# Performance work log

Measured on AMD Instinct MI355X. Metric: run time of the kernel, lower is better.

The kernel has to match this reference:

```python
import jax, jax.numpy as jnp
import numpy as np

FRAC_BITS = 16            # fixed-point fractional bits (MPC fixedpoint precision)
SCALE = float(1 << FRAC_BITS)

def fxp(v):
    """Emulate dup_with_precision: round value to the fixed-point grid with
    FRAC_BITS fractional bits. Straight-through (identity) gradient, matching
    the MPC backward pass which propagates gradients through truncation."""
    return v + jax.lax.stop_gradient(jnp.round(v * SCALE) / SCALE - v)


def setup_inputs() -> dict:
    key = jax.random.key(0)
    kx, kw = jax.random.split(key)
    in_dim, out_dim, batch = 4096, 4096, 2048
    x = jax.random.normal(kx, (batch, in_dim), dtype=jnp.float32)
    # Dense_Local init: w ~ N(0, 1/sqrt(in_dim+1)), b = zeros
    w = jax.random.normal(kw, (in_dim, out_dim), dtype=jnp.float32) / np.sqrt(in_dim + 1)
    b = jnp.zeros((out_dim,), dtype=jnp.float32)
    return {"x": x, "w": w, "b": b}


def reference(x, w, b):
    # quantize operands to the fixed-point grid (values live on the grid in MPC)
    xq = fxp(x)
    wq = fxp(w)
    # y = x @ w, then dup_with_precision(x.fixedpoint): truncate product back
    y = fxp(jnp.matmul(xq, wq))           # [batch, out_dim]
    # + bias
    y = y + fxp(b)
    # secure ReLU: s = drelu_local(y) (sign bit), y = relu(y, s) = y * s
    s = y >= 0
    y = jnp.where(s, y, jnp.zeros((), dtype=y.dtype))
    # final dup_with_precision(new_fixedpoint=x.fixedpoint)
    return fxp(y)
```

## Files before the change

### kernel.cpp

```cpp
#include <hip/hip_runtime.h>
#include <hip/hip_bf16.h>
#include <stdint.h>

#define M_DIM 2048
#define N_DIM 4096
#define K_DIM 4096

#define NT 64

typedef short short8 __attribute__((ext_vector_type(8)));
typedef float f32x4 __attribute__((ext_vector_type(4)));

typedef __attribute__((address_space(1))) unsigned int gu32;
typedef __attribute__((address_space(3))) unsigned int lu32;

__device__ static inline unsigned short f32_to_bf16(float f) {
  union { float f; unsigned int u; } v; v.f = f;
  unsigned int u = v.u;
  u += 0x7FFFu + ((u >> 16) & 1u);
  return (unsigned short)(u >> 16);
}

__global__ void cvt_x_kernel(const float* __restrict__ in, unsigned short* __restrict__ out) {
  size_t i = ((size_t)blockIdx.x * blockDim.x + threadIdx.x) * 8;
  f32x4 a = *(const f32x4*)(in + i);
  f32x4 b = *(const f32x4*)(in + i + 4);
  short8 o;
  o[0] = (short)f32_to_bf16(a[0]); o[1] = (short)f32_to_bf16(a[1]);
  o[2] = (short)f32_to_bf16(a[2]); o[3] = (short)f32_to_bf16(a[3]);
  o[4] = (short)f32_to_bf16(b[0]); o[5] = (short)f32_to_bf16(b[1]);
  o[6] = (short)f32_to_bf16(b[2]); o[7] = (short)f32_to_bf16(b[3]);
  *(short8*)(out + i) = o;
}

__global__ void transpose_cvt_w_kernel(const float* __restrict__ w, unsigned short* __restrict__ wt) {
  __shared__ unsigned short tile[64][64 + 8];
  int bn = blockIdx.x * 64;
  int bk = blockIdx.y * 64;
  int t = threadIdx.x;
  int c4 = (t & 15) * 4;
  int r0 = t >> 4;
#pragma unroll
  for (int p = 0; p < 4; ++p) {
    int r = r0 + p * 16;
    f32x4 v = *(const f32x4*)(w + (size_t)(bk + r) * N_DIM + bn + c4);
    tile[c4 + 0][r] = f32_to_bf16(v[0]);
    tile[c4 + 1][r] = f32_to_bf16(v[1]);
    tile[c4 + 2][r] = f32_to_bf16(v[2]);
    tile[c4 + 3][r] = f32_to_bf16(v[3]);
  }
  __syncthreads();
  int orow = t >> 2;
  int oc = (t & 3) * 16;
  short8 lo, hi;
#pragma unroll
  for (int j = 0; j < 8; ++j) {
    lo[j] = (short)tile[orow][oc + j];
    hi[j] = (short)tile[orow][oc + 8 + j];
  }
  unsigned short* op = wt + (size_t)(bn + orow) * K_DIM + bk + oc;
  *(short8*)(op) = lo;
  *(short8*)(op + 8) = hi;
}


__global__ __launch_bounds__(512) void gemm8_kernel(
    const unsigned short* __restrict__ A, const unsigned short* __restrict__ Bt,
    const float* __restrict__ bias, float* __restrict__ C) {
  __shared__ unsigned short sm16[3 * 24576];
  char* smem = (char*)&sm16[0];

  const int tid = threadIdx.x;
  const int lane = tid & 63;
  const int w = tid >> 6;
  const int wm = w >> 2, wn = w & 3;

  const int id = blockIdx.x;
  const int x = id & 7, j = id >> 3;
  const int by = ((x >> 2) << 3) + (j >> 2);
  const int bx = ((x & 3) << 2) + (j & 3);
  const int r0 = by * 128, c0 = bx * 256;

  const int l8 = lane >> 3, l7 = lane & 7;
  const int chunkE = ((l7 ^ (l8 & 7)) << 3);
  const unsigned short* Ag = A + (size_t)(r0 + w * 16 + l8) * K_DIM + chunkE;
  const unsigned short* Bg = Bt + (size_t)(c0 + w * 32 + l8) * K_DIM + chunkE;
  const int aL0 = w * 2048;
  const int bL0 = 16384 + w * 4096;

#define GL(gp, ldsoff) __builtin_amdgcn_global_load_lds((gu32*)(gp), (lu32*)(smem + (ldsoff)), 16, 0, 0)
#define STAGE_ALL(t, sb)                                               \
  do {                                                                 \
    GL(Ag + (size_t)(t) * 64, (sb) + aL0);                             \
    GL(Ag + (size_t)(t) * 64 + 8 * (size_t)K_DIM, (sb) + aL0 + 1024);  \
    GL(Bg + (size_t)(t) * 64, (sb) + bL0);                             \
    GL(Bg + (size_t)(t) * 64 + 8 * (size_t)K_DIM, (sb) + bL0 + 1024);  \
    GL(Bg + (size_t)(t) * 64 + 16 * (size_t)K_DIM, (sb) + bL0 + 2048); \
    GL(Bg + (size_t)(t) * 64 + 24 * (size_t)K_DIM, (sb) + bL0 + 3072); \
  } while (0)

  const int l15 = lane & 15, hi = lane >> 4;
  const int aR = (wm * 64 + l15) * 64;
  const int bR = 8192 + (wn * 64 + l15) * 64;
  const int slot0 = ((hi ^ l7) << 3);
  const int slot1 = (((4 + hi) ^ l7) << 3);

  f32x4 acc[4][4] = {};

  STAGE_ALL(0, 0);
  STAGE_ALL(1, 49152);

  int cs = 0;
  for (int t = 0; t < NT; ++t) {
    const int sE = cs * 24576;
    const int stB = (cs == 0 ? 2 : cs - 1) * 49152;
    const bool doStage = (t + 2) < NT;

    if (t < NT - 1) asm volatile("s_waitcnt vmcnt(6) lgkmcnt(0)" ::: "memory");
    else            asm volatile("s_waitcnt vmcnt(0) lgkmcnt(0)" ::: "memory");
    __builtin_amdgcn_sched_barrier(0);
    asm volatile("s_barrier" ::: "memory");

    short8 a0[4], b0[4], a1[4], b1[4];
#pragma unroll
    for (int m = 0; m < 4; ++m) a0[m] = *(const short8*)(sm16 + sE + aR + m * 1024 + slot0);
#pragma unroll
    for (int n = 0; n < 4; ++n) b0[n] = *(const short8*)(sm16 + sE + bR + n * 1024 + slot0);
    if (doStage) STAGE_ALL(t + 2, stB);
#pragma unroll
    for (int m = 0; m < 4; ++m) a1[m] = *(const short8*)(sm16 + sE + aR + m * 1024 + slot1);
#pragma unroll
    for (int n = 0; n < 4; ++n) b1[n] = *(const short8*)(sm16 + sE + bR + n * 1024 + slot1);

    __builtin_amdgcn_s_setprio(1);
#pragma unroll
    for (int m = 0; m < 4; ++m)
#pragma unroll
      for (int n = 0; n < 4; ++n)
        acc[m][n] = __builtin_amdgcn_mfma_f32_16x16x32_bf16(a0[m], b0[n], acc[m][n], 0, 0, 0);
#pragma unroll
    for (int m = 0; m < 4; ++m)
#pragma unroll
      for (int n = 0; n < 4; ++n)
        acc[m][n] = __builtin_amdgcn_mfma_f32_16x16x32_bf16(a1[m], b1[n], acc[m][n], 0, 0, 0);
    __builtin_amdgcn_s_setprio(0);

    cs = (cs == 2) ? 0 : cs + 1;
  }

  const float S = 65536.0f, IS = 1.0f / 65536.0f;
  const int lr = hi * 4;
#pragma unroll
  for (int n = 0; n < 4; ++n) {
    int gcol = c0 + wn * 64 + n * 16 + l15;
    float bq = rintf(bias[gcol] * S) * IS;
#pragma unroll
    for (int m = 0; m < 4; ++m) {
      int grow = r0 + wm * 64 + m * 16 + lr;
      float* outp = C + (size_t)grow * N_DIM + gcol;
#pragma unroll
      for (int r = 0; r < 4; ++r) {
        float t = rintf(acc[m][n][r] * S) * IS + bq;
        t = t > 0.0f ? t : 0.0f;
        outp[(size_t)r * N_DIM] = t;
      }
    }
  }
#undef GL
#undef STAGE_ALL
}

__global__ __launch_bounds__(256, 2) void gemm_fb_kernel(
    const float* __restrict__ Xf, const float* __restrict__ Wf,
    const float* __restrict__ bias, float* __restrict__ C) {
  __shared__ unsigned short As[128][64];
  __shared__ unsigned short Bs[128][64];
  int tid = threadIdx.x;
  int lane = tid & 63;
  int wid = tid >> 6;
  int wr = wid >> 1, wc = wid & 1;
  int r0 = blockIdx.y * 128;
  int c0 = blockIdx.x * 128;
  f32x4 acc[4][4] = {};
  for (int kt = 0; kt < K_DIM / 64; ++kt) {
    __syncthreads();
    int ar = tid >> 1;
    int ac = (tid & 1) * 32;
    const float* xp = Xf + (size_t)(r0 + ar) * K_DIM + kt * 64 + ac;
#pragma unroll
    for (int jj = 0; jj < 8; ++jj) {
      f32x4 v = *(const f32x4*)(xp + jj * 4);
      As[ar][ac + jj * 4 + 0] = f32_to_bf16(v[0]);
      As[ar][ac + jj * 4 + 1] = f32_to_bf16(v[1]);
      As[ar][ac + jj * 4 + 2] = f32_to_bf16(v[2]);
      As[ar][ac + jj * 4 + 3] = f32_to_bf16(v[3]);
    }
    int bk_ = tid >> 2;
    int bc = (tid & 3) * 32;
    const float* wp = Wf + (size_t)(kt * 64 + bk_) * N_DIM + c0 + bc;
#pragma unroll
    for (int jj = 0; jj < 8; ++jj) {
      f32x4 v = *(const f32x4*)(wp + jj * 4);
      Bs[bc + jj * 4 + 0][bk_] = f32_to_bf16(v[0]);
      Bs[bc + jj * 4 + 1][bk_] = f32_to_bf16(v[1]);
      Bs[bc + jj * 4 + 2][bk_] = f32_to_bf16(v[2]);
      Bs[bc + jj * 4 + 3][bk_] = f32_to_bf16(v[3]);
    }
    __syncthreads();
#pragma unroll
    for (int ks = 0; ks < 2; ++ks) {
      int co = ks * 32 + (lane >> 4) * 8;
      int rA = wr * 64 + (lane & 15);
      int rB = wc * 64 + (lane & 15);
      short8 a[4], b[4];
#pragma unroll
      for (int m = 0; m < 4; ++m) a[m] = *(const short8*)&As[rA + m * 16][co];
#pragma unroll
      for (int n = 0; n < 4; ++n) b[n] = *(const short8*)&Bs[rB + n * 16][co];
#pragma unroll
      for (int m = 0; m < 4; ++m)
#pragma unroll
        for (int n = 0; n < 4; ++n)
          acc[m][n] = __builtin_amdgcn_mfma_f32_16x16x32_bf16(a[m], b[n], acc[m][n], 0, 0, 0);
    }
  }
  const float S = 65536.0f, IS = 1.0f / 65536.0f;
  int lr = (lane >> 4) * 4;
  int lc = lane & 15;
#pragma unroll
  for (int n = 0; n < 4; ++n) {
    int gcol = c0 + wc * 64 + n * 16 + lc;
    float bq = rintf(bias[gcol] * S) * IS;
#pragma unroll
    for (int m = 0; m < 4; ++m) {
      int grow = r0 + wr * 64 + m * 16 + lr;
      float* outp = C + (size_t)grow * N_DIM + gcol;
#pragma unroll
      for (int r = 0; r < 4; ++r) {
        float t = rintf(acc[m][n][r] * S) * IS + bq;
        t = t > 0.0f ? t : 0.0f;
        outp[(size_t)r * N_DIM] = t;
      }
    }
  }
}

extern "C" void kernel_launch(void* const* d_in, const int* in_sizes, int n_in,
                              void* d_out, int out_size, void* d_ws, size_t ws_size,
                              hipStream_t stream) {
  const float* x = (const float*)d_in[0];
  const float* w = (const float*)d_in[1];
  const float* b = (const float*)d_in[2];
  float* out = (float*)d_out;

  size_t needA = (size_t)M_DIM * K_DIM * sizeof(unsigned short);
  size_t needB = (size_t)K_DIM * N_DIM * sizeof(unsigned short);

  if (ws_size >= needA + needB) {
    unsigned short* Abf = (unsigned short*)d_ws;
    unsigned short* Btbf = (unsigned short*)((char*)d_ws + needA);
    cvt_x_kernel<<<(M_DIM * (size_t)K_DIM / 8 + 255) / 256, 256, 0, stream>>>(x, Abf);
    transpose_cvt_w_kernel<<<dim3(N_DIM / 64, K_DIM / 64), 256, 0, stream>>>(w, Btbf);
    gemm8_kernel<<<256, 512, 0, stream>>>(Abf, Btbf, b, out);
  } else {
    gemm_fb_kernel<<<dim3(N_DIM / 128, M_DIM / 128), 256, 0, stream>>>(x, w, b, out);
  }
}
```

Before: 90.88 us.

## Pre-pack W into MFMA fragment layout and load B directly to registers

The weight conversion kernel now writes W as bf16 in a per-wave MFMA fragment order instead of a plain transpose. The GEMM loads B fragments straight from global memory into registers, double-buffered across two unrolled tiles, and only stages A through LDS. This cuts LDS capacity and traffic and removes the B LDS reads. In exchange, each wave issues its own B global loads, and B is no longer shared through LDS across the two wm waves, so global and L2 traffic for B roughly doubles and latency must be hidden by register prefetch.

```diff
diff --git a/kernel.cpp b/kernel.cpp
--- a/kernel.cpp
+++ b/kernel.cpp
@@ -33,42 +33,41 @@
   *(short8*)(out + i) = o;
 }
 
-__global__ void transpose_cvt_w_kernel(const float* __restrict__ w, unsigned short* __restrict__ wt) {
-  __shared__ unsigned short tile[64][64 + 8];
+__global__ void bfrag_w_kernel(const float* __restrict__ w, unsigned short* __restrict__ bf) {
+  __shared__ unsigned short tile2[64][72];
   int bn = blockIdx.x * 64;
   int bk = blockIdx.y * 64;
   int t = threadIdx.x;
   int c4 = (t & 15) * 4;
-  int r0 = t >> 4;
+  int r0t = t >> 4;
 #pragma unroll
   for (int p = 0; p < 4; ++p) {
-    int r = r0 + p * 16;
+    int r = r0t + p * 16;
     f32x4 v = *(const f32x4*)(w + (size_t)(bk + r) * N_DIM + bn + c4);
-    tile[c4 + 0][r] = f32_to_bf16(v[0]);
-    tile[c4 + 1][r] = f32_to_bf16(v[1]);
-    tile[c4 + 2][r] = f32_to_bf16(v[2]);
-    tile[c4 + 3][r] = f32_to_bf16(v[3]);
+    tile2[c4 + 0][r] = f32_to_bf16(v[0]);
+    tile2[c4 + 1][r] = f32_to_bf16(v[1]);
+    tile2[c4 + 2][r] = f32_to_bf16(v[2]);
+    tile2[c4 + 3][r] = f32_to_bf16(v[3]);
   }
   __syncthreads();
-  int orow = t >> 2;
-  int oc = (t & 3) * 16;
-  short8 lo, hi;
-#pragma unroll
-  for (int j = 0; j < 8; ++j) {
-    lo[j] = (short)tile[orow][oc + j];
-    hi[j] = (short)tile[orow][oc + 8 + j];
-  }
-  unsigned short* op = wt + (size_t)(bn + orow) * K_DIM + bk + oc;
-  *(short8*)(op) = lo;
-  *(short8*)(op + 8) = hi;
+#pragma unroll
+  for (int pass = 0; pass < 2; ++pass) {
+    int u = t + pass * 256;
+    int ngL = u >> 7;
+    int off = u & 127;
+    int ch = off >> 4, l = off & 15;
+    short8 val = *(const short8*)&tile2[ngL * 16 + l][ch * 8];
+    size_t base = ((size_t)((bn >> 4) + ngL) * 64 + (size_t)(bk >> 6)) * 2048;
+    *(short8*)((char*)bf + base + (size_t)off * 16) = val;
+  }
 }
 
 
 __global__ __launch_bounds__(512) void gemm8_kernel(
-    const unsigned short* __restrict__ A, const unsigned short* __restrict__ Bt,
+    const unsigned short* __restrict__ A, const char* __restrict__ Bfrag,
     const float* __restrict__ bias, float* __restrict__ C) {
-  __shared__ unsigned short sm16[3 * 24576];
-  char* smem = (char*)&sm16[0];
+  __shared__ unsigned short smA[3 * 8192];
+  char* smemc = (char*)&smA[0];
 
   const int tid = threadIdx.x;
   const int lane = tid & 63;
@@ -82,70 +81,71 @@
   const int r0 = by * 128, c0 = bx * 256;
 
   const int l8 = lane >> 3, l7 = lane & 7;
-  const int chunkE = ((l7 ^ (l8 & 7)) << 3);
+  const int chunkE = ((l7 ^ l8) << 3);
   const unsigned short* Ag = A + (size_t)(r0 + w * 16 + l8) * K_DIM + chunkE;
-  const unsigned short* Bg = Bt + (size_t)(c0 + w * 32 + l8) * K_DIM + chunkE;
   const int aL0 = w * 2048;
-  const int bL0 = 16384 + w * 4096;
-
-#define GL(gp, ldsoff) __builtin_amdgcn_global_load_lds((gu32*)(gp), (lu32*)(smem + (ldsoff)), 16, 0, 0)
-#define STAGE_ALL(t, sb)                                               \
-  do {                                                                 \
-    GL(Ag + (size_t)(t) * 64, (sb) + aL0);                             \
-    GL(Ag + (size_t)(t) * 64 + 8 * (size_t)K_DIM, (sb) + aL0 + 1024);  \
-    GL(Bg + (size_t)(t) * 64, (sb) + bL0);                             \
-    GL(Bg + (size_t)(t) * 64 + 8 * (size_t)K_DIM, (sb) + bL0 + 1024);  \
-    GL(Bg + (size_t)(t) * 64 + 16 * (size_t)K_DIM, (sb) + bL0 + 2048); \
-    GL(Bg + (size_t)(t) * 64 + 24 * (size_t)K_DIM, (sb) + bL0 + 3072); \
+
+#define GL(gp, ldsoff) __builtin_amdgcn_global_load_lds((gu32*)(gp), (lu32*)(smemc + (ldsoff)), 16, 0, 0)
+#define STAGE_A(t, sb)                                                \
+  do {                                                                \
+    GL(Ag + (size_t)(t) * 64, (sb) + aL0);                            \
+    GL(Ag + (size_t)(t) * 64 + 8 * (size_t)K_DIM, (sb) + aL0 + 1024); \
   } while (0)
+
+  const int ngBase = (c0 >> 4) + wn * 4;
+  const char* Bb = Bfrag + (size_t)ngBase * 64 * 2048 + (size_t)lane * 16;
 
   const int l15 = lane & 15, hi = lane >> 4;
   const int aR = (wm * 64 + l15) * 64;
-  const int bR = 8192 + (wn * 64 + l15) * 64;
   const int slot0 = ((hi ^ l7) << 3);
   const int slot1 = (((4 + hi) ^ l7) << 3);
 
   f32x4 acc[4][4] = {};
-
-  STAGE_ALL(0, 0);
-  STAGE_ALL(1, 49152);
+  short8 bE[4][2], bO[4][2];
+
+  STAGE_A(0, 0);
+#pragma unroll
+  for (int n = 0; n < 4; ++n) {
+    bE[n][0] = *(const short8*)(Bb + (size_t)n * 131072);
+    bE[n][1] = *(const short8*)(Bb + (size_t)n * 131072 + 1024);
+  }
+  STAGE_A(1, 16384);
+
+#define TILE_BODY(T, BCUR, BNXT)                                                                  \
+  {                                                                                               \
+    const int sE = cs * 8192;                                                                     \
+    const int stB = (cs == 0 ? 2 : cs - 1) * 16384;                                               \
+    if ((T) < NT - 1) asm volatile("s_waitcnt vmcnt(2) lgkmcnt(0)" ::: "memory");                 \
+    else              asm volatile("s_waitcnt vmcnt(0) lgkmcnt(0)" ::: "memory");                 \
+    __builtin_amdgcn_sched_barrier(0);                                                            \
+    asm volatile("s_barrier" ::: "memory");                                                       \
+    if ((T) + 1 < NT) {                                                                           \
+      _Pragma("unroll") for (int n = 0; n < 4; ++n) {                                             \
+        BNXT[n][0] = *(const short8*)(Bb + (size_t)n * 131072 + (size_t)((T) + 1) * 2048);        \
+        BNXT[n][1] = *(const short8*)(Bb + (size_t)n * 131072 + (size_t)((T) + 1) * 2048 + 1024); \
+      }                                                                                           \
+    }                                                                                             \
+    if ((T) + 2 < NT) { STAGE_A((T) + 2, stB); }                                                  \
+    short8 a0[4], a1[4];                                                                          \
+    _Pragma("unroll") for (int m = 0; m < 4; ++m)                                                 \
+        a0[m] = *(const short8*)(smA + sE + aR + m * 1024 + slot0);                               \
+    _Pragma("unroll") for (int m = 0; m < 4; ++m)                                                 \
+        a1[m] = *(const short8*)(smA + sE + aR + m * 1024 + slot1);                               \
+    __builtin_amdgcn_s_setprio(1);                                                                \
+    _Pragma("unroll") for (int m = 0; m < 4; ++m)                                                 \
+      _Pragma("unroll") for (int n = 0; n < 4; ++n)                                               \
+          acc[m][n] = __builtin_amdgcn_mfma_f32_16x16x32_bf16(a0[m], BCUR[n][0], acc[m][n], 0, 0, 0); \
+    _Pragma("unroll") for (int m = 0; m < 4; ++m)                                                 \
+      _Pragma("unroll") for (int n = 0; n < 4; ++n)                                               \
+          acc[m][n] = __builtin_amdgcn_mfma_f32_16x16x32_bf16(a1[m], BCUR[n][1], acc[m][n], 0, 0, 0); \
+    __builtin_amdgcn_s_setprio(0);                                                                \
+    cs = (cs == 2) ? 0 : cs + 1;                                                                  \
+  }
 
   int cs = 0;
-  for (int t = 0; t < NT; ++t) {
-    const int sE = cs * 24576;
-    const int stB = (cs == 0 ? 2 : cs - 1) * 49152;
-    const bool doStage = (t + 2) < NT;
-
-    if (t < NT - 1) asm volatile("s_waitcnt vmcnt(6) lgkmcnt(0)" ::: "memory");
-    else            asm volatile("s_waitcnt vmcnt(0) lgkmcnt(0)" ::: "memory");
-    __builtin_amdgcn_sched_barrier(0);
-    asm volatile("s_barrier" ::: "memory");
-
-    short8 a0[4], b0[4], a1[4], b1[4];
-#pragma unroll
-    for (int m = 0; m < 4; ++m) a0[m] = *(const short8*)(sm16 + sE + aR + m * 1024 + slot0);
-#pragma unroll
-    for (int n = 0; n < 4; ++n) b0[n] = *(const short8*)(sm16 + sE + bR + n * 1024 + slot0);
-    if (doStage) STAGE_ALL(t + 2, stB);
-#pragma unroll
-    for (int m = 0; m < 4; ++m) a1[m] = *(const short8*)(sm16 + sE + aR + m * 1024 + slot1);
-#pragma unroll
-    for (int n = 0; n < 4; ++n) b1[n] = *(const short8*)(sm16 + sE + bR + n * 1024 + slot1);
-
-    __builtin_amdgcn_s_setprio(1);
-#pragma unroll
-    for (int m = 0; m < 4; ++m)
-#pragma unroll
-      for (int n = 0; n < 4; ++n)
-        acc[m][n] = __builtin_amdgcn_mfma_f32_16x16x32_bf16(a0[m], b0[n], acc[m][n], 0, 0, 0);
-#pragma unroll
-    for (int m = 0; m < 4; ++m)
-#pragma unroll
-      for (int n = 0; n < 4; ++n)
-        acc[m][n] = __builtin_amdgcn_mfma_f32_16x16x32_bf16(a1[m], b1[n], acc[m][n], 0, 0, 0);
-    __builtin_amdgcn_s_setprio(0);
-
-    cs = (cs == 2) ? 0 : cs + 1;
+  for (int t2 = 0; t2 < NT; t2 += 2) {
+    TILE_BODY(t2, bE, bO);
+    TILE_BODY(t2 + 1, bO, bE);
   }
 
   const float S = 65536.0f, IS = 1.0f / 65536.0f;
@@ -167,7 +167,8 @@
     }
   }
 #undef GL
-#undef STAGE_ALL
+#undef STAGE_A
+#undef TILE_BODY
 }
 
 __global__ __launch_bounds__(256, 2) void gemm_fb_kernel(
@@ -258,10 +259,10 @@
 
   if (ws_size >= needA + needB) {
     unsigned short* Abf = (unsigned short*)d_ws;
-    unsigned short* Btbf = (unsigned short*)((char*)d_ws + needA);
+    unsigned short* Bfr = (unsigned short*)((char*)d_ws + needA);
     cvt_x_kernel<<<(M_DIM * (size_t)K_DIM / 8 + 255) / 256, 256, 0, stream>>>(x, Abf);
-    transpose_cvt_w_kernel<<<dim3(N_DIM / 64, K_DIM / 64), 256, 0, stream>>>(w, Btbf);
-    gemm8_kernel<<<256, 512, 0, stream>>>(Abf, Btbf, b, out);
+    bfrag_w_kernel<<<dim3(N_DIM / 64, K_DIM / 64), 256, 0, stream>>>(w, Bfr);
+    gemm8_kernel<<<256, 512, 0, stream>>>(Abf, (const char*)Bfr, b, out);
   } else {
     gemm_fb_kernel<<<dim3(N_DIM / 128, M_DIM / 128), 256, 0, stream>>>(x, w, b, out);
   }
```

Measured after the change: 103.3 us. 1.14x slower.

## Use 4-wave GEMM blocks with 64x128 per-wave tiles and split LDS reads

Applied to the files above, without the earlier changes.

Drops the GEMM block from 8 waves to 4, keeping the 128x256 block tile, so each wave now computes a 64x128 sub-tile with 32 accumulators. Each wave issues twice as many async global-to-LDS loads per stage, and the vmcnt wait is raised to match. LDS fragment reads are split into two halves, with the second half read after the first MFMA group, to overlap LDS latency with compute. The aim is more register-level operand reuse and fewer LDS reads per MFMA. The cost is far higher register pressure and less wave-level parallelism for hiding latency.

```diff
diff --git a/kernel.cpp b/kernel.cpp
--- a/kernel.cpp
+++ b/kernel.cpp
@@ -64,16 +64,16 @@
 }
 
 
-__global__ __launch_bounds__(512) void gemm8_kernel(
+__global__ __launch_bounds__(256, 1) void gemm4_kernel(
     const unsigned short* __restrict__ A, const unsigned short* __restrict__ Bt,
     const float* __restrict__ bias, float* __restrict__ C) {
-  __shared__ unsigned short sm16[3 * 24576];
-  char* smem = (char*)&sm16[0];
+  __shared__ unsigned short smA[3 * 24576];
+  char* smemc = (char*)&smA[0];
 
   const int tid = threadIdx.x;
   const int lane = tid & 63;
   const int w = tid >> 6;
-  const int wm = w >> 2, wn = w & 3;
+  const int wm = w >> 1, wn = w & 1;
 
   const int id = blockIdx.x;
   const int x = id & 7, j = id >> 3;
@@ -82,66 +82,67 @@
   const int r0 = by * 128, c0 = bx * 256;
 
   const int l8 = lane >> 3, l7 = lane & 7;
-  const int chunkE = ((l7 ^ (l8 & 7)) << 3);
-  const unsigned short* Ag = A + (size_t)(r0 + w * 16 + l8) * K_DIM + chunkE;
-  const unsigned short* Bg = Bt + (size_t)(c0 + w * 32 + l8) * K_DIM + chunkE;
-  const int aL0 = w * 2048;
-  const int bL0 = 16384 + w * 4096;
-
-#define GL(gp, ldsoff) __builtin_amdgcn_global_load_lds((gu32*)(gp), (lu32*)(smem + (ldsoff)), 16, 0, 0)
-#define STAGE_ALL(t, sb)                                               \
-  do {                                                                 \
-    GL(Ag + (size_t)(t) * 64, (sb) + aL0);                             \
-    GL(Ag + (size_t)(t) * 64 + 8 * (size_t)K_DIM, (sb) + aL0 + 1024);  \
-    GL(Bg + (size_t)(t) * 64, (sb) + bL0);                             \
-    GL(Bg + (size_t)(t) * 64 + 8 * (size_t)K_DIM, (sb) + bL0 + 1024);  \
-    GL(Bg + (size_t)(t) * 64 + 16 * (size_t)K_DIM, (sb) + bL0 + 2048); \
-    GL(Bg + (size_t)(t) * 64 + 24 * (size_t)K_DIM, (sb) + bL0 + 3072); \
-  } while (0)
+  const int chunkE = ((l7 ^ l8) << 3);
+  const unsigned short* Ag = A + (size_t)(r0 + w * 32 + l8) * K_DIM + chunkE;
+  const unsigned short* Bg = Bt + (size_t)(c0 + w * 64 + l8) * K_DIM + chunkE;
+
+#define GL(gp, ldsoff) __builtin_amdgcn_global_load_lds((gu32*)(gp), (lu32*)(smemc + (ldsoff)), 16, 0, 0)
+  auto STAGE = [&](int T, int sb) {
+#pragma unroll
+    for (int i = 0; i < 4; ++i)
+      GL(Ag + (size_t)T * 64 + (size_t)i * 8 * K_DIM, sb + w * 4096 + i * 1024);
+#pragma unroll
+    for (int i = 0; i < 8; ++i)
+      GL(Bg + (size_t)T * 64 + (size_t)i * 8 * K_DIM, sb + 16384 + w * 8192 + i * 1024);
+  };
 
   const int l15 = lane & 15, hi = lane >> 4;
   const int aR = (wm * 64 + l15) * 64;
-  const int bR = 8192 + (wn * 64 + l15) * 64;
+  const int bR = 8192 + (wn * 128 + l15) * 64;
   const int slot0 = ((hi ^ l7) << 3);
   const int slot1 = (((4 + hi) ^ l7) << 3);
 
-  f32x4 acc[4][4] = {};
-
-  STAGE_ALL(0, 0);
-  STAGE_ALL(1, 49152);
+  f32x4 acc[4][8] = {};
+
+  STAGE(0, 0);
+  STAGE(1, 49152);
 
   int cs = 0;
   for (int t = 0; t < NT; ++t) {
     const int sE = cs * 24576;
     const int stB = (cs == 0 ? 2 : cs - 1) * 49152;
-    const bool doStage = (t + 2) < NT;
-
-    if (t < NT - 1) asm volatile("s_waitcnt vmcnt(6) lgkmcnt(0)" ::: "memory");
+
+    if (t < NT - 1) asm volatile("s_waitcnt vmcnt(12) lgkmcnt(0)" ::: "memory");
     else            asm volatile("s_waitcnt vmcnt(0) lgkmcnt(0)" ::: "memory");
     __builtin_amdgcn_sched_barrier(0);
     asm volatile("s_barrier" ::: "memory");
 
-    short8 a0[4], b0[4], a1[4], b1[4];
-#pragma unroll
-    for (int m = 0; m < 4; ++m) a0[m] = *(const short8*)(sm16 + sE + aR + m * 1024 + slot0);
-#pragma unroll
-    for (int n = 0; n < 4; ++n) b0[n] = *(const short8*)(sm16 + sE + bR + n * 1024 + slot0);
-    if (doStage) STAGE_ALL(t + 2, stB);
-#pragma unroll
-    for (int m = 0; m < 4; ++m) a1[m] = *(const short8*)(sm16 + sE + aR + m * 1024 + slot1);
-#pragma unroll
-    for (int n = 0; n < 4; ++n) b1[n] = *(const short8*)(sm16 + sE + bR + n * 1024 + slot1);
+    short8 a0[4], b0[8];
+#pragma unroll
+    for (int m = 0; m < 4; ++m) a0[m] = *(const short8*)(smA + sE + aR + m * 1024 + slot0);
+#pragma unroll
+    for (int n = 0; n < 8; ++n) b0[n] = *(const short8*)(smA + sE + bR + n * 1024 + slot0);
+    if (t + 2 < NT) STAGE(t + 2, stB);
 
     __builtin_amdgcn_s_setprio(1);
 #pragma unroll
     for (int m = 0; m < 4; ++m)
 #pragma unroll
-      for (int n = 0; n < 4; ++n)
+      for (int n = 0; n < 8; ++n)
         acc[m][n] = __builtin_amdgcn_mfma_f32_16x16x32_bf16(a0[m], b0[n], acc[m][n], 0, 0, 0);
+    __builtin_amdgcn_s_setprio(0);
+
+    short8 a1[4], b1[8];
+#pragma unroll
+    for (int m = 0; m < 4; ++m) a1[m] = *(const short8*)(smA + sE + aR + m * 1024 + slot1);
+#pragma unroll
+    for (int n = 0; n < 8; ++n) b1[n] = *(const short8*)(smA + sE + bR + n * 1024 + slot1);
+
+    __builtin_amdgcn_s_setprio(1);
 #pragma unroll
     for (int m = 0; m < 4; ++m)
 #pragma unroll
-      for (int n = 0; n < 4; ++n)
+      for (int n = 0; n < 8; ++n)
         acc[m][n] = __builtin_amdgcn_mfma_f32_16x16x32_bf16(a1[m], b1[n], acc[m][n], 0, 0, 0);
     __builtin_amdgcn_s_setprio(0);
 
@@ -151,8 +152,8 @@
   const float S = 65536.0f, IS = 1.0f / 65536.0f;
   const int lr = hi * 4;
 #pragma unroll
-  for (int n = 0; n < 4; ++n) {
-    int gcol = c0 + wn * 64 + n * 16 + l15;
+  for (int n = 0; n < 8; ++n) {
+    int gcol = c0 + wn * 128 + n * 16 + l15;
     float bq = rintf(bias[gcol] * S) * IS;
 #pragma unroll
     for (int m = 0; m < 4; ++m) {
@@ -167,7 +168,6 @@
     }
   }
 #undef GL
-#undef STAGE_ALL
 }
 
 __global__ __launch_bounds__(256, 2) void gemm_fb_kernel(
@@ -261,7 +261,7 @@
     unsigned short* Btbf = (unsigned short*)((char*)d_ws + needA);
     cvt_x_kernel<<<(M_DIM * (size_t)K_DIM / 8 + 255) / 256, 256, 0, stream>>>(x, Abf);
     transpose_cvt_w_kernel<<<dim3(N_DIM / 64, K_DIM / 64), 256, 0, stream>>>(w, Btbf);
-    gemm8_kernel<<<256, 512, 0, stream>>>(Abf, Btbf, b, out);
+    gemm4_kernel<<<256, 256, 0, stream>>>(Abf, Btbf, b, out);
   } else {
     gemm_fb_kernel<<<dim3(N_DIM / 128, M_DIM / 128), 256, 0, stream>>>(x, w, b, out);
   }
```

New measurement: 95.81 us. 5.4% more time.

## Split K across wave halves with larger per-wave tiles and LDS reduction

Applied to the files above, without the earlier changes.

Instead of 8 waves each owning a distinct 64x64 output tile over the full K slice, waves are split into two halves that each handle half of each 64-wide K step, with each wave computing a 64x128 tile (4x8 accumulators). The partial sums from the second half are exchanged through LDS and added by the first half before the epilogue. The goal is fewer LDS reads per MFMA, since each A/B fragment is reused across more outputs. The cost is twice the accumulator registers, which may lower occupancy or cause spills, plus an extra LDS reduction pass and idle waves during the epilogue.

```diff
diff --git a/kernel.cpp b/kernel.cpp
--- a/kernel.cpp
+++ b/kernel.cpp
@@ -67,13 +67,15 @@
 __global__ __launch_bounds__(512) void gemm8_kernel(
     const unsigned short* __restrict__ A, const unsigned short* __restrict__ Bt,
     const float* __restrict__ bias, float* __restrict__ C) {
-  __shared__ unsigned short sm16[3 * 24576];
-  char* smem = (char*)&sm16[0];
+  __shared__ unsigned short smA[3 * 24576];
+  char* smemc = (char*)&smA[0];
 
   const int tid = threadIdx.x;
   const int lane = tid & 63;
   const int w = tid >> 6;
-  const int wm = w >> 2, wn = w & 3;
+  const int q = w & 3;
+  const int half = w >> 2;
+  const int qm = q >> 1, qn = q & 1;
 
   const int id = blockIdx.x;
   const int x = id & 7, j = id >> 3;
@@ -82,13 +84,13 @@
   const int r0 = by * 128, c0 = bx * 256;
 
   const int l8 = lane >> 3, l7 = lane & 7;
-  const int chunkE = ((l7 ^ (l8 & 7)) << 3);
+  const int chunkE = ((l7 ^ l8) << 3);
   const unsigned short* Ag = A + (size_t)(r0 + w * 16 + l8) * K_DIM + chunkE;
   const unsigned short* Bg = Bt + (size_t)(c0 + w * 32 + l8) * K_DIM + chunkE;
   const int aL0 = w * 2048;
   const int bL0 = 16384 + w * 4096;
 
-#define GL(gp, ldsoff) __builtin_amdgcn_global_load_lds((gu32*)(gp), (lu32*)(smem + (ldsoff)), 16, 0, 0)
+#define GL(gp, ldsoff) __builtin_amdgcn_global_load_lds((gu32*)(gp), (lu32*)(smemc + (ldsoff)), 16, 0, 0)
 #define STAGE_ALL(t, sb)                                               \
   do {                                                                 \
     GL(Ag + (size_t)(t) * 64, (sb) + aL0);                             \
@@ -100,69 +102,80 @@
   } while (0)
 
   const int l15 = lane & 15, hi = lane >> 4;
-  const int aR = (wm * 64 + l15) * 64;
-  const int bR = 8192 + (wn * 64 + l15) * 64;
-  const int slot0 = ((hi ^ l7) << 3);
-  const int slot1 = (((4 + hi) ^ l7) << 3);
-
-  f32x4 acc[4][4] = {};
+  const int aR = (qm * 64 + l15) * 64;
+  const int bR = 8192 + (qn * 128 + l15) * 64;
+  const int slotH = (((half << 2) + hi) ^ l7) << 3;
+  const unsigned short* pA0 = smA + 0 * 24576 + aR + slotH;
+  const unsigned short* pA1 = smA + 1 * 24576 + aR + slotH;
+  const unsigned short* pA2 = smA + 2 * 24576 + aR + slotH;
+  const unsigned short* pB0 = smA + 0 * 24576 + bR + slotH;
+  const unsigned short* pB1 = smA + 1 * 24576 + bR + slotH;
+  const unsigned short* pB2 = smA + 2 * 24576 + bR + slotH;
+
+  f32x4 acc[4][8] = {};
 
   STAGE_ALL(0, 0);
   STAGE_ALL(1, 49152);
 
   int cs = 0;
   for (int t = 0; t < NT; ++t) {
-    const int sE = cs * 24576;
     const int stB = (cs == 0 ? 2 : cs - 1) * 49152;
     const bool doStage = (t + 2) < NT;
 
+    const unsigned short* pAs = (cs == 0) ? pA0 : (cs == 1) ? pA1 : pA2;
+    const unsigned short* pBs = (cs == 0) ? pB0 : (cs == 1) ? pB1 : pB2;
+
     if (t < NT - 1) asm volatile("s_waitcnt vmcnt(6) lgkmcnt(0)" ::: "memory");
     else            asm volatile("s_waitcnt vmcnt(0) lgkmcnt(0)" ::: "memory");
-    __builtin_amdgcn_sched_barrier(0);
     asm volatile("s_barrier" ::: "memory");
 
-    short8 a0[4], b0[4], a1[4], b1[4];
-#pragma unroll
-    for (int m = 0; m < 4; ++m) a0[m] = *(const short8*)(sm16 + sE + aR + m * 1024 + slot0);
-#pragma unroll
-    for (int n = 0; n < 4; ++n) b0[n] = *(const short8*)(sm16 + sE + bR + n * 1024 + slot0);
+    short8 a[4], b[8];
+#pragma unroll
+    for (int m = 0; m < 4; ++m) a[m] = *(const short8*)(pAs + m * 1024);
+#pragma unroll
+    for (int n = 0; n < 8; ++n) b[n] = *(const short8*)(pBs + n * 1024);
     if (doStage) STAGE_ALL(t + 2, stB);
-#pragma unroll
-    for (int m = 0; m < 4; ++m) a1[m] = *(const short8*)(sm16 + sE + aR + m * 1024 + slot1);
-#pragma unroll
-    for (int n = 0; n < 4; ++n) b1[n] = *(const short8*)(sm16 + sE + bR + n * 1024 + slot1);
 
     __builtin_amdgcn_s_setprio(1);
 #pragma unroll
     for (int m = 0; m < 4; ++m)
 #pragma unroll
-      for (int n = 0; n < 4; ++n)
-        acc[m][n] = __builtin_amdgcn_mfma_f32_16x16x32_bf16(a0[m], b0[n], acc[m][n], 0, 0, 0);
+      for (int n = 0; n < 8; ++n)
+        acc[m][n] = __builtin_amdgcn_mfma_f32_16x16x32_bf16(a[m], b[n], acc[m][n], 0, 0, 0);
+    __builtin_amdgcn_s_setprio(0);
+
+    cs = (cs == 2) ? 0 : cs + 1;
+  }
+
+  __syncthreads();
+  float* xch = (float*)&smA[0];
+  if (half == 1) {
 #pragma unroll
     for (int m = 0; m < 4; ++m)
 #pragma unroll
-      for (int n = 0; n < 4; ++n)
-        acc[m][n] = __builtin_amdgcn_mfma_f32_16x16x32_bf16(a1[m], b1[n], acc[m][n], 0, 0, 0);
-    __builtin_amdgcn_s_setprio(0);
-
-    cs = (cs == 2) ? 0 : cs + 1;
-  }
-
-  const float S = 65536.0f, IS = 1.0f / 65536.0f;
-  const int lr = hi * 4;
-#pragma unroll
-  for (int n = 0; n < 4; ++n) {
-    int gcol = c0 + wn * 64 + n * 16 + l15;
-    float bq = rintf(bias[gcol] * S) * IS;
-#pragma unroll
-    for (int m = 0; m < 4; ++m) {
-      int grow = r0 + wm * 64 + m * 16 + lr;
-      float* outp = C + (size_t)grow * N_DIM + gcol;
-#pragma unroll
-      for (int r = 0; r < 4; ++r) {
-        float t = rintf(acc[m][n][r] * S) * IS + bq;
-        t = t > 0.0f ? t : 0.0f;
-        outp[(size_t)r * N_DIM] = t;
+      for (int n = 0; n < 8; ++n)
+        *(f32x4*)(xch + q * 8192 + (m * 8 + n) * 256 + lane * 4) = acc[m][n];
+  }
+  __syncthreads();
+
+  if (half == 0) {
+    const float S = 65536.0f, IS = 1.0f / 65536.0f;
+    const int lr = hi * 4;
+#pragma unroll
+    for (int n = 0; n < 8; ++n) {
+      int gcol = c0 + qn * 128 + n * 16 + l15;
+      float bq = rintf(bias[gcol] * S) * IS;
+#pragma unroll
+      for (int m = 0; m < 4; ++m) {
+        f32x4 part = *(const f32x4*)(xch + q * 8192 + (m * 8 + n) * 256 + lane * 4);
+        int grow = r0 + qm * 64 + m * 16 + lr;
+        float* outp = C + (size_t)grow * N_DIM + gcol;
+#pragma unroll
+        for (int r = 0; r < 4; ++r) {
+          float t = rintf((acc[m][n][r] + part[r]) * S) * IS + bq;
+          t = t > 0.0f ? t : 0.0f;
+          outp[(size_t)r * N_DIM] = t;
+        }
       }
     }
   }
```

Result: faster. 89.00 us (-2.1%).
